# Kernel tuning notes

Hardware: AMD Instinct MI355X
Metric: run time of the kernel (lower is better)

## Reference

```python
import jax, jax.numpy as jnp
import numpy as np

N_SENT = 262144
N_BAGS = 4096
HIDDEN = 256
HIER = 2
LAYER0 = 14
NUM_CLASSES = 53


def setup_inputs() -> dict:
    key = jax.random.key(0)
    ks = jax.random.split(key, 8)
    x = jax.random.normal(ks[0], (N_SENT, HIDDEN), dtype=jnp.float32)
    rel_emb0 = jax.random.normal(ks[1], (LAYER0, HIDDEN), dtype=jnp.float32) * 0.1
    rel_emb1 = jax.random.normal(ks[2], (NUM_CLASSES, HIDDEN), dtype=jnp.float32) * 0.1
    disc = jax.random.normal(ks[3], (NUM_CLASSES, 2 * HIDDEN), dtype=jnp.float32) * 0.05
    bias = jnp.zeros((NUM_CLASSES,), dtype=jnp.float32)
    # relation_levels[r] = (coarse node id, fine node id) for relation r
    relation_levels = jnp.stack(
        [jax.random.randint(ks[4], (NUM_CLASSES,), 0, LAYER0, dtype=jnp.int32),
         jnp.arange(NUM_CLASSES, dtype=jnp.int32)], axis=1)
    label_index = jax.random.randint(ks[5], (N_SENT,), 0, NUM_CLASSES, dtype=jnp.int32)
    # ragged bag boundaries: scope[0]=0, scope[-1]=N_SENT, interior sorted
    interior = jnp.sort(jax.random.randint(ks[6], (N_BAGS - 1,), 1, N_SENT, dtype=jnp.int32))
    scope = jnp.concatenate([jnp.zeros((1,), jnp.int32), interior,
                             jnp.full((1,), N_SENT, jnp.int32)])
    return {"x": x, "rel_emb0": rel_emb0, "rel_emb1": rel_emb1, "disc": disc,
            "bias": bias, "relation_levels": relation_levels,
            "label_index": label_index, "scope": scope}


def _segment_ids(scope, n):
    # scope: [B+1] sorted boundaries -> per-sentence bag id [n]
    marks = jnp.zeros((n,), jnp.int32).at[scope[1:-1]].add(1)
    return jnp.cumsum(marks)


def reference(x, rel_emb0, rel_emb1, disc, bias, relation_levels, label_index, scope):
    n = x.shape[0]
    b = scope.shape[0] - 1
    seg = _segment_ids(scope, n)                       # [N]
    ll = relation_levels[label_index]                  # [N, 2]
    # per-level attention logits: <rel_emb[level][node], x>
    lg0 = jnp.sum(rel_emb0[ll[:, 0]] * x, axis=-1)     # [N]
    lg1 = jnp.sum(rel_emb1[ll[:, 1]] * x, axis=-1)     # [N]
    logits = jnp.stack([lg0, lg1], axis=1)             # [N, hier]
    # ragged softmax per bag (stable)
    m = jax.ops.segment_max(logits, seg, num_segments=b)     # [B, hier]
    e = jnp.exp(logits - m[seg])
    s = jax.ops.segment_sum(e, seg, num_segments=b)          # [B, hier]
    score = e / s[seg]                                       # [N, hier]
    # attention-weighted sentence reduction per bag per level
    weighted = score[:, :, None] * x[:, None, :]             # [N, hier, H]
    repre = jax.ops.segment_sum(weighted, seg, num_segments=b)  # [B, hier, H]
    stack_repre = repre.reshape(b, HIER * HIDDEN)            # [B, 2H]
    return stack_repre @ disc.T + bias                       # [B, 53]
```

## Files before the change

### kernel.cpp

```cpp
#include <hip/hip_runtime.h>
#include <math.h>

#define HIDDEN 256
#define NUM_CLASSES 53
#define CHUNK 64


__global__ __launch_bounds__(256) void k0_init(
    const int* __restrict__ scope, int* __restrict__ seg,
    float* __restrict__ repre, float* __restrict__ s)
{
    const int b = blockIdx.x;
    const int t = threadIdx.x;
    repre[(size_t)b * 512 + t]       = 0.f;
    repre[(size_t)b * 512 + 256 + t] = 0.f;
    if (t < 2) s[2 * b + t] = 0.f;
    const int st = scope[b], en = scope[b + 1];
    for (int i = st + t; i < en; i += 256) seg[i] = b;
}

__global__ __launch_bounds__(256) void k1_main(
    const float* __restrict__ x,
    const float* __restrict__ rel_emb0,
    const float* __restrict__ rel_emb1,
    const int* __restrict__ relation_levels,
    const int* __restrict__ label_index,
    const int* __restrict__ seg,
    float* __restrict__ repre,
    float* __restrict__ s)
{
    const int c0   = blockIdx.x * CHUNK;
    const int tid  = threadIdx.x;
    const int lane = tid & 63;
    const int wave = tid >> 6;
    const int half = lane >> 5;
    const int j    = lane & 31;
    const int colb = j * 8;
    const int stream = wave * 2 + half;

    __shared__ float e_lds[CHUNK][2];
    __shared__ int   s_seg[CHUNK];

    if (tid < CHUNK) s_seg[tid] = seg[c0 + tid];

    #pragma unroll
    for (int k = 0; k < CHUNK / 8; ++k) {
        const int row = c0 + 8 * k + stream;
        const float* xp = x + (size_t)row * HIDDEN + colb;
        const float4 xa = *reinterpret_cast<const float4*>(xp);
        const float4 xb = *reinterpret_cast<const float4*>(xp + 4);
        const int lbl = label_index[row];
        const int2 rl = *reinterpret_cast<const int2*>(relation_levels + 2 * lbl);
        const float* p0 = rel_emb0 + (size_t)rl.x * HIDDEN + colb;
        const float* p1 = rel_emb1 + (size_t)rl.y * HIDDEN + colb;
        const float4 r0a = *reinterpret_cast<const float4*>(p0);
        const float4 r0b = *reinterpret_cast<const float4*>(p0 + 4);
        const float4 r1a = *reinterpret_cast<const float4*>(p1);
        const float4 r1b = *reinterpret_cast<const float4*>(p1 + 4);

        float lg0 = xa.x*r0a.x + xa.y*r0a.y + xa.z*r0a.z + xa.w*r0a.w
                  + xb.x*r0b.x + xb.y*r0b.y + xb.z*r0b.z + xb.w*r0b.w;
        float lg1 = xa.x*r1a.x + xa.y*r1a.y + xa.z*r1a.z + xa.w*r1a.w
                  + xb.x*r1b.x + xb.y*r1b.y + xb.z*r1b.z + xb.w*r1b.w;

        #pragma unroll
        for (int off = 16; off > 0; off >>= 1) {
            lg0 += __shfl_xor(lg0, off, 64);
            lg1 += __shfl_xor(lg1, off, 64);
        }
        if (j == 0) {
            e_lds[8 * k + stream][0] = __expf(lg0);
            e_lds[8 * k + stream][1] = __expf(lg1);
        }
    }
    __syncthreads();

    float acc0 = 0.f, acc1 = 0.f, se0 = 0.f, se1 = 0.f;
    int curbag = s_seg[0];
    for (int r = 0; r < CHUNK; ++r) {
        const float e0 = e_lds[r][0];
        const float e1 = e_lds[r][1];
        const float xv = x[(size_t)(c0 + r) * HIDDEN + tid];
        acc0 += e0 * xv;
        acc1 += e1 * xv;
        se0  += e0;
        se1  += e1;
        const bool last = (r == CHUNK - 1);
        if (last || s_seg[r + 1] != curbag) {
            atomicAdd(&repre[(size_t)curbag * 512 + tid],       acc0);
            atomicAdd(&repre[(size_t)curbag * 512 + 256 + tid], acc1);
            if (tid == 0) atomicAdd(&s[2 * curbag],     se0);
            if (tid == 1) atomicAdd(&s[2 * curbag + 1], se1);
            acc0 = acc1 = se0 = se1 = 0.f;
            if (!last) curbag = s_seg[r + 1];
        }
    }
}

__global__ __launch_bounds__(256) void k2_head(
    const float* __restrict__ repre,
    const float* __restrict__ s,
    const float* __restrict__ disc,
    const float* __restrict__ bias,
    float* __restrict__ out)
{
    const int tid  = threadIdx.x;
    const int lane = tid & 63;
    const int wave = tid >> 6;
    const int bag  = blockIdx.x * 4 + wave;

    __shared__ float s_rep[4][2 * HIDDEN];

    const float s0 = s[2 * bag], s1 = s[2 * bag + 1];
    const float inv0 = (s0 > 0.f) ? 1.f / s0 : 0.f;
    const float inv1 = (s1 > 0.f) ? 1.f / s1 : 0.f;
    const float inv  = (lane < 32) ? inv0 : inv1;

    const float4* rp = reinterpret_cast<const float4*>(repre + (size_t)bag * 512 + lane * 8);
    float4 v0 = rp[0], v1 = rp[1];
    v0.x *= inv; v0.y *= inv; v0.z *= inv; v0.w *= inv;
    v1.x *= inv; v1.y *= inv; v1.z *= inv; v1.w *= inv;
    float4* dst = reinterpret_cast<float4*>(&s_rep[wave][lane * 8]);
    dst[0] = v0; dst[1] = v1;

    if (lane < NUM_CLASSES) {
        const float4* dr = reinterpret_cast<const float4*>(disc + (size_t)lane * 512);
        const float4* rr = reinterpret_cast<const float4*>(s_rep[wave]);
        float p = 0.f;
        #pragma unroll 8
        for (int k = 0; k < 128; ++k) {
            const float4 d = dr[k];
            const float4 r = rr[k];
            p += d.x * r.x + d.y * r.y + d.z * r.z + d.w * r.w;
        }
        out[bag * NUM_CLASSES + lane] = p + bias[lane];
    }
}

extern "C" void kernel_launch(void* const* d_in, const int* in_sizes, int n_in,
                              void* d_out, int out_size, void* d_ws, size_t ws_size,
                              hipStream_t stream) {
    const float* x               = (const float*)d_in[0];
    const float* rel_emb0        = (const float*)d_in[1];
    const float* rel_emb1        = (const float*)d_in[2];
    const float* disc            = (const float*)d_in[3];
    const float* bias            = (const float*)d_in[4];
    const int*   relation_levels = (const int*)d_in[5];
    const int*   label_index     = (const int*)d_in[6];
    const int*   scope           = (const int*)d_in[7];
    float*       out             = (float*)d_out;

    const int n_bags = in_sizes[7] - 1;
    const int n_rows = in_sizes[6];

    float* repre = (float*)d_ws;
    float* s_ws  = repre + (size_t)n_bags * 512;
    int*   seg   = (int*)(s_ws + 2 * n_bags);

    k0_init<<<n_bags, 256, 0, stream>>>(scope, seg, repre, s_ws);
    k1_main<<<n_rows / CHUNK, 256, 0, stream>>>(
        x, rel_emb0, rel_emb1, relation_levels, label_index, seg, repre, s_ws);
    k2_head<<<n_bags / 4, 256, 0, stream>>>(repre, s_ws, disc, bias, out);
}
```

Baseline: 482.3 us.

## Accumulate weighted rows in registers and reduce per-bag partials through LDS slots

Each half-wave now handles 8 consecutive rows and accumulates exp-weighted x directly in registers from the values already loaded for the logit dot product, instead of re-reading x from global memory in a second pass. Per-bag partials are merged through shared-memory atomics into a small set of LDS slots, then written to global with one atomicAdd per slot, with a global-atomic fallback for bags beyond the slot range. This removes the second read of x and the serial 64-row loop, at the cost of about 20KB of LDS per block, LDS initialisation and atomic contention, and a launch-bounds occupancy hint.

```diff
diff --git a/kernel.cpp b/kernel.cpp
--- a/kernel.cpp
+++ b/kernel.cpp
@@ -4,6 +4,7 @@
 #define HIDDEN 256
 #define NUM_CLASSES 53
 #define CHUNK 64
+#define NSLOT 10
 
 
 __global__ __launch_bounds__(256) void k0_init(
@@ -19,7 +20,7 @@
     for (int i = st + t; i < en; i += 256) seg[i] = b;
 }
 
-__global__ __launch_bounds__(256) void k1_main(
+__global__ __launch_bounds__(256, 4) void k1_main(
     const float* __restrict__ x,
     const float* __restrict__ rel_emb0,
     const float* __restrict__ rel_emb1,
@@ -37,15 +38,59 @@
     const int j    = lane & 31;
     const int colb = j * 8;
     const int stream = wave * 2 + half;
-
-    __shared__ float e_lds[CHUNK][2];
+    const int r0 = c0 + 8 * stream;
+
     __shared__ int   s_seg[CHUNK];
-
+    __shared__ float s_acc[NSLOT][2][HIDDEN];
+    __shared__ float s_sum[NSLOT][2];
+    __shared__ int   s_used[NSLOT];
+
+    for (int t = tid; t < NSLOT * 2 * HIDDEN; t += 256)
+        (&s_acc[0][0][0])[t] = 0.f;
+    if (tid < NSLOT) { s_used[tid] = 0; s_sum[tid][0] = 0.f; s_sum[tid][1] = 0.f; }
     if (tid < CHUNK) s_seg[tid] = seg[c0 + tid];
-
+    __syncthreads();
+    const int seg0 = s_seg[0];
+
+    float a0[8], a1[8];
     #pragma unroll
-    for (int k = 0; k < CHUNK / 8; ++k) {
-        const int row = c0 + 8 * k + stream;
+    for (int k = 0; k < 8; ++k) { a0[k] = 0.f; a1[k] = 0.f; }
+    float se0 = 0.f, se1 = 0.f;
+    int cur = s_seg[8 * stream];
+
+    auto flush_seg = [&](int bag) {
+        const int sl = bag - seg0;
+        if (sl < NSLOT) {
+            #pragma unroll
+            for (int k = 0; k < 8; ++k) {
+                atomicAdd(&s_acc[sl][0][colb + k], a0[k]);
+                atomicAdd(&s_acc[sl][1][colb + k], a1[k]);
+            }
+            if (j == 0) {
+                atomicAdd(&s_sum[sl][0], se0);
+                atomicAdd(&s_sum[sl][1], se1);
+                s_used[sl] = 1;
+            }
+        } else {
+            const size_t base = (size_t)bag * 512;
+            #pragma unroll
+            for (int k = 0; k < 8; ++k) {
+                atomicAdd(&repre[base + colb + k],       a0[k]);
+                atomicAdd(&repre[base + 256 + colb + k], a1[k]);
+            }
+            if (j == 0) {
+                atomicAdd(&s[2 * bag],     se0);
+                atomicAdd(&s[2 * bag + 1], se1);
+            }
+        }
+        #pragma unroll
+        for (int k = 0; k < 8; ++k) { a0[k] = 0.f; a1[k] = 0.f; }
+        se0 = 0.f; se1 = 0.f;
+    };
+
+    #pragma unroll
+    for (int r = 0; r < 8; ++r) {
+        const int row = r0 + r;
         const float* xp = x + (size_t)row * HIDDEN + colb;
         const float4 xa = *reinterpret_cast<const float4*>(xp);
         const float4 xb = *reinterpret_cast<const float4*>(xp + 4);
@@ -68,31 +113,33 @@
             lg0 += __shfl_xor(lg0, off, 64);
             lg1 += __shfl_xor(lg1, off, 64);
         }
-        if (j == 0) {
-            e_lds[8 * k + stream][0] = __expf(lg0);
-            e_lds[8 * k + stream][1] = __expf(lg1);
-        }
+        const float e0 = __expf(lg0);
+        const float e1 = __expf(lg1);
+
+        const int bg = s_seg[8 * stream + r];
+        if (bg != cur) { flush_seg(cur); cur = bg; }
+
+        a0[0] += e0 * xa.x;  a0[1] += e0 * xa.y;
+        a0[2] += e0 * xa.z;  a0[3] += e0 * xa.w;
+        a0[4] += e0 * xb.x;  a0[5] += e0 * xb.y;
+        a0[6] += e0 * xb.z;  a0[7] += e0 * xb.w;
+        a1[0] += e1 * xa.x;  a1[1] += e1 * xa.y;
+        a1[2] += e1 * xa.z;  a1[3] += e1 * xa.w;
+        a1[4] += e1 * xb.x;  a1[5] += e1 * xb.y;
+        a1[6] += e1 * xb.z;  a1[7] += e1 * xb.w;
+        se0 += e0;
+        se1 += e1;
     }
+    flush_seg(cur);
     __syncthreads();
 
-    float acc0 = 0.f, acc1 = 0.f, se0 = 0.f, se1 = 0.f;
-    int curbag = s_seg[0];
-    for (int r = 0; r < CHUNK; ++r) {
-        const float e0 = e_lds[r][0];
-        const float e1 = e_lds[r][1];
-        const float xv = x[(size_t)(c0 + r) * HIDDEN + tid];
-        acc0 += e0 * xv;
-        acc1 += e1 * xv;
-        se0  += e0;
-        se1  += e1;
-        const bool last = (r == CHUNK - 1);
-        if (last || s_seg[r + 1] != curbag) {
-            atomicAdd(&repre[(size_t)curbag * 512 + tid],       acc0);
-            atomicAdd(&repre[(size_t)curbag * 512 + 256 + tid], acc1);
-            if (tid == 0) atomicAdd(&s[2 * curbag],     se0);
-            if (tid == 1) atomicAdd(&s[2 * curbag + 1], se1);
-            acc0 = acc1 = se0 = se1 = 0.f;
-            if (!last) curbag = s_seg[r + 1];
+    for (int sl = 0; sl < NSLOT; ++sl) {
+        if (s_used[sl]) {
+            const size_t base = (size_t)(seg0 + sl) * 512;
+            atomicAdd(&repre[base + tid],       s_acc[sl][0][tid]);
+            atomicAdd(&repre[base + 256 + tid], s_acc[sl][1][tid]);
+            if (tid == 0) atomicAdd(&s[2 * (seg0 + sl)],     s_sum[sl][0]);
+            if (tid == 1) atomicAdd(&s[2 * (seg0 + sl) + 1], s_sum[sl][1]);
         }
     }
 }
```

After: 500.3 us. 1.04x slower.
